# Performance work log

Hardware: AMD Instinct MI355X
Metric: run time of the kernel (lower is better)

Reference implementation:

```python
import jax, jax.numpy as jnp
import numpy as np

NUM_HEADS = 16


def setup_inputs() -> dict:
    key = jax.random.key(0)
    ks = jax.random.split(key, 8)
    B, S, H = 2, 2048, 1024
    sd = 1.0 / np.sqrt(H)
    return {
        "x": jax.random.normal(ks[0], (B, S, H), dtype=jnp.float32),
        "mask": jax.random.randint(ks[1], (B, S), 0, 2, dtype=jnp.int32),
        "wq": jax.random.normal(ks[2], (H, H), dtype=jnp.float32) * sd,
        "bq": jnp.zeros((H,), jnp.float32),
        "wk": jax.random.normal(ks[3], (H, H), dtype=jnp.float32) * sd,
        "bk": jnp.zeros((H,), jnp.float32),
        "wv": jax.random.normal(ks[4], (H, H), dtype=jnp.float32) * sd,
        "bv": jnp.zeros((H,), jnp.float32),
        "wo": jax.random.normal(ks[5], (H, H), dtype=jnp.float32) * sd,
        "bo": jnp.zeros((H,), jnp.float32),
        "wg": jax.random.normal(ks[6], (H, H), dtype=jnp.float32) * sd,
        "bg": jnp.zeros((H,), jnp.float32),
    }


def reference(x, mask, wq, bq, wk, bk, wv, bv, wo, bo, wg, bg):
    B, S, H = x.shape
    nh = NUM_HEADS
    hd = H // nh
    scale = hd ** -0.5

    def split_heads(t):  # [B,S,H] -> [B,nh,S,hd]
        return t.reshape(B, S, nh, hd).transpose(0, 2, 1, 3)

    q = split_heads(x @ wq.T + bq)
    k = split_heads(x @ wk.T + bk)
    v = split_heads(x @ wv.T + bv)

    scores = jnp.einsum("bhqd,bhkd->bhqk", q, k) * scale
    # key-padding mask broadcast to [B,1,1,S]
    scores = jnp.where(mask[:, None, None, :] == 0, jnp.float32(-10000.0), scores)
    attn_weights = jax.nn.softmax(scores, axis=-1)  # dropout is identity in eval

    context = jnp.einsum("bhqk,bhkd->bhqd", attn_weights, v)
    context = context.transpose(0, 2, 1, 3).reshape(B, S, H)

    gate_values = jax.nn.sigmoid(context @ wg.T + bg)
    output = (context @ wo.T + bo) * gate_values
    return output, attn_weights
```

## Files before the change

### kernel.cpp

```cpp
#include <hip/hip_runtime.h>
#include <math.h>

#define BB 2
#define SS 2048
#define HH 1024
#define NH 16
#define HD 64
#define LDK 40

typedef __attribute__((ext_vector_type(8))) short short8;
typedef __attribute__((ext_vector_type(4))) float floatx4;

__device__ __forceinline__ unsigned short f2bf(float f) {
    unsigned u = __float_as_uint(f);
    u += 0x7FFF + ((u >> 16) & 1);
    return (unsigned short)(u >> 16);
}
__device__ __forceinline__ float bf2f(unsigned short h) {
    return __uint_as_float((unsigned)h << 16);
}

struct SplitJob { const float* src; unsigned short* dh; unsigned short* dl; int n; };
struct SplitJobs { SplitJob j[6]; };

__global__ __launch_bounds__(256) void presplit(SplitJobs jobs)
{
    SplitJob jb = jobs.j[blockIdx.y];
    const int i = (blockIdx.x * 256 + threadIdx.x) * 8;
    if (i >= jb.n) return;
    float4 v0 = *(const float4*)(jb.src + i);
    float4 v1 = *(const float4*)(jb.src + i + 4);
    float f[8] = {v0.x, v0.y, v0.z, v0.w, v1.x, v1.y, v1.z, v1.w};
    union { unsigned short s[8]; uint4 v; } h, l;
#pragma unroll
    for (int j = 0; j < 8; ++j) {
        const unsigned short hs = f2bf(f[j]);
        h.s[j] = hs;
        l.s[j] = f2bf(f[j] - bf2f(hs));
    }
    *(uint4*)(jb.dh + i) = h.v;
    *(uint4*)(jb.dl + i) = l.v;
}

__global__ __launch_bounds__(256) void rs_reduce(
    const float* __restrict__ part, float* __restrict__ inv)
{
    const int i = blockIdx.x * 256 + threadIdx.x;
    const int zz = i >> 11, row = i & 2047;
    const float* p = part + (size_t)zz * 32 * SS + row;
    float s = 0.f;
#pragma unroll
    for (int nb = 0; nb < 32; ++nb) s += p[(size_t)nb * SS];
    inv[i] = 1.0f / s;
}

__global__ __launch_bounds__(256) void vtranspose_bf(
    const unsigned short* __restrict__ Vh, const unsigned short* __restrict__ Vl,
    unsigned short* __restrict__ VTh, unsigned short* __restrict__ VTl)
{
    __shared__ __attribute__((aligned(16))) unsigned short t[64][72];
    const int zz = blockIdx.z;
    const int b = zz >> 1;
    const unsigned short* V = (zz & 1) ? Vl : Vh;
    unsigned short* VT = (zz & 1) ? VTl : VTh;
    const int k0 = blockIdx.x * 64;
    const int h = blockIdx.y;
    const int tid = threadIdx.x;
    {
        const int row = tid >> 2, c0 = (tid & 3) * 16;
        const int sw = ((row >> 4) & 3) << 4;
        const unsigned short* g = V + (size_t)(b * SS + k0 + row) * (3 * HH) + h * HD + c0;
        uint4 u0 = *(const uint4*)g;
        uint4 u1 = *(const uint4*)(g + 8);
        *(uint4*)&t[row][c0 ^ sw] = u0;
        *(uint4*)&t[row][(c0 ^ sw) + 8] = u1;
    }
    __syncthreads();
    {
        const int d = tid >> 2, kq = tid & 3;
        const int cs = d ^ (kq << 4);
        union { unsigned short s[16]; uint4 v[2]; } o;
#pragma unroll
        for (int i = 0; i < 16; ++i) o.s[i] = t[kq * 16 + i][cs];
        unsigned short* p = VT + ((size_t)(b * NH + h) * HD + d) * SS + k0 + kq * 16;
        *(uint4*)p = o.v[0];
        *(uint4*)(p + 8) = o.v[1];
    }
}

template<int BN, int MODE>
__global__ __launch_bounds__(256) void gemm_bf(
    const unsigned short* __restrict__ Ah, const unsigned short* __restrict__ Al,
    float* __restrict__ Af,
    const unsigned short* __restrict__ Bh, const unsigned short* __restrict__ Bl,
    const unsigned short* __restrict__ B2h, const unsigned short* __restrict__ B2l,
    const float* __restrict__ bias, const float* __restrict__ bias2, const float* __restrict__ bias3,
    float* __restrict__ Cf, unsigned short* __restrict__ Ch, unsigned short* __restrict__ Cl,
    const float* __restrict__ rs_in, float* __restrict__ rs_out,
    const int* __restrict__ mask,
    int K, int lda, int ldb, int ldc,
    long long sAb, long long sAh, long long sBb, long long sBh,
    long long sCb, long long sCh)
{
    constexpr int BM = 128;
    constexpr int MT = 4;
    constexpr int NT = BN / 32;
    constexpr int NSET = (MODE == 3) ? 2 : 1;

    __shared__ __attribute__((aligned(16))) unsigned short AhS[BM * LDK];
    __shared__ __attribute__((aligned(16))) unsigned short AlS[BM * LDK];
    __shared__ __attribute__((aligned(16))) unsigned short BhS[NSET * BN * LDK];
    __shared__ __attribute__((aligned(16))) unsigned short BlS[NSET * BN * LDK];

    const int tid  = threadIdx.x;
    const int lane = tid & 63;
    const int wave = tid >> 6;
    const int wm = wave >> 1, wn = wave & 1;
    const int r16 = lane & 15, quad = lane >> 4;

    const int z  = blockIdx.z;
    const int bz = z >> 4, hz = z & 15;

    const int m0 = blockIdx.y * BM;
    const int n0 = blockIdx.x * BN;

    floatx4 acc[MT][NT][NSET];
#pragma unroll
    for (int mt = 0; mt < MT; ++mt)
#pragma unroll
        for (int nt = 0; nt < NT; ++nt)
#pragma unroll
            for (int s = 0; s < NSET; ++s)
                acc[mt][nt][s] = (floatx4){0.f, 0.f, 0.f, 0.f};

    const int arow = tid >> 1, ac = (tid & 1) * 16;
    const int brow = (BN == 128) ? (tid >> 1) : (tid >> 2);
    const int bc   = (BN == 128) ? ((tid & 1) * 16) : ((tid & 3) * 8);

    const unsigned short* aph = nullptr;
    const unsigned short* apl = nullptr;
    const unsigned int*   apu = nullptr;
    float* apw = nullptr;
    float invs = 0.f;
    if constexpr (MODE == 2) {
        const size_t zo = (size_t)((long long)bz * sAb + (long long)hz * sAh);
        apu = (const unsigned int*)Af + zo + (size_t)(m0 + arow) * lda + ac;
        apw = Af + zo + (size_t)(m0 + arow) * lda + ac;
        invs = rs_in[(size_t)z * SS + m0 + arow];
    } else {
        const size_t ao = (size_t)((long long)bz * sAb + (long long)hz * sAh)
                        + (size_t)(m0 + arow) * lda + ac;
        aph = Ah + ao;
        apl = Al + ao;
    }
    const size_t boff = (size_t)((long long)bz * sBb + (long long)hz * sBh)
                      + (size_t)(n0 + brow) * ldb + bc;
    const unsigned short* bph = Bh + boff;
    const unsigned short* bpl = Bl + boff;
    const unsigned short* b2ph = nullptr;
    const unsigned short* b2pl = nullptr;
    if constexpr (MODE == 3) {
        const size_t b2o = (size_t)(n0 + brow) * ldb + bc;
        b2ph = B2h + b2o;
        b2pl = B2l + b2o;
    }

    for (int kb = 0; kb < K; kb += 32) {
        uint4 avh0, avh1, avl0, avl1;
        unsigned int uu[16];
        unsigned int hu[8], lu[8];
        uint4 bvh0, bvh1, bvl0, bvl1, cvh0, cvl0;
        if constexpr (MODE == 2) {
            uint4 u0 = *(const uint4*)(apu + kb);
            uint4 u1 = *(const uint4*)(apu + kb + 4);
            uint4 u2 = *(const uint4*)(apu + kb + 8);
            uint4 u3 = *(const uint4*)(apu + kb + 12);
            uu[0]=u0.x;  uu[1]=u0.y;  uu[2]=u0.z;  uu[3]=u0.w;
            uu[4]=u1.x;  uu[5]=u1.y;  uu[6]=u1.z;  uu[7]=u1.w;
            uu[8]=u2.x;  uu[9]=u2.y;  uu[10]=u2.z; uu[11]=u2.w;
            uu[12]=u3.x; uu[13]=u3.y; uu[14]=u3.z; uu[15]=u3.w;
        } else {
            avh0 = *(const uint4*)(aph + kb);
            avh1 = *(const uint4*)(aph + kb + 8);
            avl0 = *(const uint4*)(apl + kb);
            avl1 = *(const uint4*)(apl + kb + 8);
        }
        bvh0 = *(const uint4*)(bph + kb);
        bvl0 = *(const uint4*)(bpl + kb);
        if constexpr (BN == 128) {
            bvh1 = *(const uint4*)(bph + kb + 8);
            bvl1 = *(const uint4*)(bpl + kb + 8);
        }
        if constexpr (MODE == 3) {
            cvh0 = *(const uint4*)(b2ph + kb);
            cvl0 = *(const uint4*)(b2pl + kb);
        }
        if constexpr (MODE == 2) {
#pragma unroll
            for (int i = 0; i < 4; ++i) {
                float4 wv;
                wv.x = (__uint_as_float(uu[4*i+0] << 16) + __uint_as_float(uu[4*i+0] & 0xffff0000u)) * invs;
                wv.y = (__uint_as_float(uu[4*i+1] << 16) + __uint_as_float(uu[4*i+1] & 0xffff0000u)) * invs;
                wv.z = (__uint_as_float(uu[4*i+2] << 16) + __uint_as_float(uu[4*i+2] & 0xffff0000u)) * invs;
                wv.w = (__uint_as_float(uu[4*i+3] << 16) + __uint_as_float(uu[4*i+3] & 0xffff0000u)) * invs;
                *(float4*)(apw + kb + i * 4) = wv;
            }
#pragma unroll
            for (int j = 0; j < 8; ++j) {
                const unsigned int a = uu[2*j], b = uu[2*j+1];
                hu[j] = (a & 0xffffu) | (b << 16);
                lu[j] = (a >> 16) | (b & 0xffff0000u);
            }
        }
        __syncthreads();
        if constexpr (MODE == 2) {
            uint4 t0, t1, t2, t3;
            t0.x=hu[0]; t0.y=hu[1]; t0.z=hu[2]; t0.w=hu[3];
            t1.x=hu[4]; t1.y=hu[5]; t1.z=hu[6]; t1.w=hu[7];
            t2.x=lu[0]; t2.y=lu[1]; t2.z=lu[2]; t2.w=lu[3];
            t3.x=lu[4]; t3.y=lu[5]; t3.z=lu[6]; t3.w=lu[7];
            *(uint4*)&AhS[arow * LDK + ac]     = t0;
            *(uint4*)&AhS[arow * LDK + ac + 8] = t1;
            *(uint4*)&AlS[arow * LDK + ac]     = t2;
            *(uint4*)&AlS[arow * LDK + ac + 8] = t3;
        } else {
            *(uint4*)&AhS[arow * LDK + ac]     = avh0;
            *(uint4*)&AhS[arow * LDK + ac + 8] = avh1;
            *(uint4*)&AlS[arow * LDK + ac]     = avl0;
            *(uint4*)&AlS[arow * LDK + ac + 8] = avl1;
        }
        *(uint4*)&BhS[brow * LDK + bc] = bvh0;
        *(uint4*)&BlS[brow * LDK + bc] = bvl0;
        if constexpr (BN == 128) {
            *(uint4*)&BhS[brow * LDK + bc + 8] = bvh1;
            *(uint4*)&BlS[brow * LDK + bc + 8] = bvl1;
        }
        if constexpr (MODE == 3) {
            *(uint4*)&BhS[BN * LDK + brow * LDK + bc] = cvh0;
            *(uint4*)&BlS[BN * LDK + brow * LDK + bc] = cvl0;
        }
        __syncthreads();

        short8 fah[MT], fal[MT], fbh[NSET][NT], fbl[NSET][NT];
#pragma unroll
        for (int mt = 0; mt < MT; ++mt) {
            const int rr = (wm * 64 + mt * 16 + r16) * LDK + quad * 8;
            fah[mt] = *(const short8*)&AhS[rr];
            fal[mt] = *(const short8*)&AlS[rr];
        }
#pragma unroll
        for (int s = 0; s < NSET; ++s)
#pragma unroll
            for (int nt = 0; nt < NT; ++nt) {
                const int rr = s * BN * LDK + (wn * (BN / 2) + nt * 16 + r16) * LDK + quad * 8;
                fbh[s][nt] = *(const short8*)&BhS[rr];
                fbl[s][nt] = *(const short8*)&BlS[rr];
            }
#pragma unroll
        for (int mt = 0; mt < MT; ++mt)
#pragma unroll
            for (int nt = 0; nt < NT; ++nt)
#pragma unroll
                for (int s = 0; s < NSET; ++s) {
                    acc[mt][nt][s] = __builtin_amdgcn_mfma_f32_16x16x32_bf16(fah[mt], fbh[s][nt], acc[mt][nt][s], 0, 0, 0);
                    acc[mt][nt][s] = __builtin_amdgcn_mfma_f32_16x16x32_bf16(fah[mt], fbl[s][nt], acc[mt][nt][s], 0, 0, 0);
                    acc[mt][nt][s] = __builtin_amdgcn_mfma_f32_16x16x32_bf16(fal[mt], fbh[s][nt], acc[mt][nt][s], 0, 0, 0);
                }
    }

    if constexpr (MODE == 0 || MODE == 2) {
        unsigned short* Chb = Ch + (size_t)((long long)bz * sCb + (long long)hz * sCh);
        unsigned short* Clb = Cl + (size_t)((long long)bz * sCb + (long long)hz * sCh);
#pragma unroll
        for (int nt = 0; nt < NT; ++nt) {
            const int col = n0 + wn * (BN / 2) + nt * 16 + r16;
            float bval = 0.f;
            if constexpr (MODE == 0) {
                const int seg = col >> 10;
                const float* bp = (seg == 0) ? bias : ((seg == 1) ? bias2 : bias3);
                bval = bp[col & (HH - 1)];
            }
#pragma unroll
            for (int mt = 0; mt < MT; ++mt) {
                const int rowb = m0 + wm * 64 + mt * 16 + quad * 4;
#pragma unroll
                for (int r = 0; r < 4; ++r) {
                    float v = acc[mt][nt][0][r];
                    if constexpr (MODE == 0) v += bval;
                    if constexpr (MODE == 2) v *= rs_in[(size_t)z * SS + rowb + r];
                    const unsigned short hv = f2bf(v);
                    const size_t idx = (size_t)(rowb + r) * ldc + col;
                    Chb[idx] = hv;
                    Clb[idx] = f2bf(v - bf2f(hv));
                }
            }
        }
    }
    if constexpr (MODE == 1) {
        unsigned int* Cbu = (unsigned int*)Cf + (size_t)((long long)bz * sCb + (long long)hz * sCh);
        float rsum[MT][4];
#pragma unroll
        for (int mt = 0; mt < MT; ++mt)
#pragma unroll
            for (int r = 0; r < 4; ++r) rsum[mt][r] = 0.f;
#pragma unroll
        for (int nt = 0; nt < NT; ++nt) {
            const int col = n0 + wn * (BN / 2) + nt * 16 + r16;
            const int mv = mask[bz * SS + col];
#pragma unroll
            for (int mt = 0; mt < MT; ++mt) {
                const int rowb = m0 + wm * 64 + mt * 16 + quad * 4;
#pragma unroll
                for (int r = 0; r < 4; ++r) {
                    const float e = mv ? __expf(acc[mt][nt][0][r] * 0.125f) : 0.f;
                    const unsigned short hv = f2bf(e);
                    const unsigned short lv = f2bf(e - bf2f(hv));
                    Cbu[(size_t)(rowb + r) * ldc + col] = (unsigned int)hv | ((unsigned int)lv << 16);
                    rsum[mt][r] += e;
                }
            }
        }
#pragma unroll
        for (int mt = 0; mt < MT; ++mt)
#pragma unroll
            for (int r = 0; r < 4; ++r) {
                float sv = rsum[mt][r];
                sv += __shfl_xor(sv, 1);
                sv += __shfl_xor(sv, 2);
                sv += __shfl_xor(sv, 4);
                sv += __shfl_xor(sv, 8);
                if (r16 == 0)
                    rs_out[((size_t)z * 32 + blockIdx.x * 2 + wn) * SS
                           + (m0 + wm * 64 + mt * 16 + quad * 4 + r)] = sv;
            }
    }
    if constexpr (MODE == 3) {
#pragma unroll
        for (int nt = 0; nt < NT; ++nt) {
            const int col = n0 + wn * (BN / 2) + nt * 16 + r16;
            const float bov = bias[col], bgv = bias2[col];
#pragma unroll
            for (int mt = 0; mt < MT; ++mt) {
                const int rowb = m0 + wm * 64 + mt * 16 + quad * 4;
#pragma unroll
                for (int r = 0; r < 4; ++r) {
                    const float o = acc[mt][nt][0][r] + bov;
                    const float g = acc[mt][nt][1][r] + bgv;
                    Cf[(size_t)(rowb + r) * ldc + col] = o / (1.f + __expf(-g));
                }
            }
        }
    }
}

extern "C" void kernel_launch(void* const* d_in, const int* in_sizes, int n_in,
                              void* d_out, int out_size, void* d_ws, size_t ws_size,
                              hipStream_t stream)
{
    const float* x    = (const float*)d_in[0];
    const int*   mask = (const int*)d_in[1];
    const float* wq = (const float*)d_in[2];  const float* bq = (const float*)d_in[3];
    const float* wk = (const float*)d_in[4];  const float* bk = (const float*)d_in[5];
    const float* wv = (const float*)d_in[6];  const float* bv = (const float*)d_in[7];
    const float* wo = (const float*)d_in[8];  const float* bo = (const float*)d_in[9];
    const float* wg = (const float*)d_in[10]; const float* bg = (const float*)d_in[11];

    const int M = BB * SS;
    const size_t NTOK = (size_t)M * HH;
    const size_t W1   = (size_t)HH * HH;
    const size_t QKVE = (size_t)M * 3 * HH;

    float* out_main = (float*)d_out;
    float* attn     = (float*)d_out + NTOK;

    unsigned short* p = (unsigned short*)d_ws;
    unsigned short* xh   = p;  p += NTOK;
    unsigned short* xl   = p;  p += NTOK;
    unsigned short* Wqh  = p;  p += 3 * W1;
    unsigned short* Wql  = p;  p += 3 * W1;
    unsigned short* Wgh  = p;  p += 2 * W1;
    unsigned short* Wgl  = p;  p += 2 * W1;
    unsigned short* QKVh = p;  p += QKVE;
    unsigned short* QKVl = p;  p += QKVE;
    unsigned short* VTh  = p;  p += NTOK;
    unsigned short* VTl  = p;  p += NTOK;

    unsigned short* CTXh = xh;
    unsigned short* CTXl = xl;
    float* rs_part = (float*)Wqh;
    float* rs_inv  = rs_part + (size_t)32 * 32 * SS;

    SplitJobs jobs;
    jobs.j[0] = SplitJob{x,  xh,           xl,           (int)NTOK};
    jobs.j[1] = SplitJob{wq, Wqh,          Wql,          (int)W1};
    jobs.j[2] = SplitJob{wk, Wqh + W1,     Wql + W1,     (int)W1};
    jobs.j[3] = SplitJob{wv, Wqh + 2 * W1, Wql + 2 * W1, (int)W1};
    jobs.j[4] = SplitJob{wo, Wgh,          Wgl,          (int)W1};
    jobs.j[5] = SplitJob{wg, Wgh + W1,     Wgl + W1,     (int)W1};
    presplit<<<dim3(2048, 6, 1), 256, 0, stream>>>(jobs);

    gemm_bf<128, 0><<<dim3(24, 32, 1), 256, 0, stream>>>(
        xh, xl, nullptr,
        Wqh, Wql, nullptr, nullptr,
        bq, bk, bv,
        nullptr, QKVh, QKVl,
        nullptr, nullptr, nullptr,
        HH, HH, HH, 3 * HH,
        0, 0, 0, 0, 0, 0);

    vtranspose_bf<<<dim3(SS / 64, NH, 2 * BB), 256, 0, stream>>>(
        QKVh + 2 * HH, QKVl + 2 * HH, VTh, VTl);

    gemm_bf<128, 1><<<dim3(16, 16, 32), 256, 0, stream>>>(
        QKVh, QKVl, nullptr,
        QKVh + HH, QKVl + HH, nullptr, nullptr,
        nullptr, nullptr, nullptr,
        attn, nullptr, nullptr,
        nullptr, rs_part, mask,
        HD, 3 * HH, 3 * HH, SS,
        (long long)SS * 3 * HH, HD, (long long)SS * 3 * HH, HD,
        (long long)NH * SS * SS, (long long)SS * SS);

    rs_reduce<<<dim3(32 * SS / 256, 1, 1), 256, 0, stream>>>(rs_part, rs_inv);

    gemm_bf<64, 2><<<dim3(1, 16, 32), 256, 0, stream>>>(
        nullptr, nullptr, attn,
        VTh, VTl, nullptr, nullptr,
        nullptr, nullptr, nullptr,
        nullptr, CTXh, CTXl,
        rs_inv, nullptr, nullptr,
        SS, SS, SS, HH,
        (long long)NH * SS * SS, (long long)SS * SS,
        (long long)NH * HD * SS, (long long)HD * SS,
        (long long)SS * HH, HD);

    gemm_bf<64, 3><<<dim3(16, 32, 1), 256, 0, stream>>>(
        CTXh, CTXl, nullptr,
        Wgh, Wgl, Wgh + W1, Wgl + W1,
        bo, bg, nullptr,
        out_main, nullptr, nullptr,
        nullptr, nullptr, nullptr,
        HH, HH, HH, HH,
        0, 0, 0, 0, 0, 0);

    (void)in_sizes; (void)n_in; (void)out_size; (void)ws_size;
}
```

Before: 1.143 ms.

## Fuse QK^T, softmax and PV into a two-pass attention kernel

```diff
diff --git a/kernel.cpp b/kernel.cpp
--- a/kernel.cpp
+++ b/kernel.cpp
@@ -18,6 +18,11 @@
 }
 __device__ __forceinline__ float bf2f(unsigned short h) {
     return __uint_as_float((unsigned)h << 16);
+}
+__device__ __forceinline__ short8 mkshort8(unsigned d0, unsigned d1, unsigned d2, unsigned d3) {
+    union { unsigned u[4]; short8 s; } t;
+    t.u[0] = d0; t.u[1] = d1; t.u[2] = d2; t.u[3] = d3;
+    return t.s;
 }
 
 struct SplitJob { const float* src; unsigned short* dh; unsigned short* dl; int n; };
@@ -40,18 +45,6 @@
     }
     *(uint4*)(jb.dh + i) = h.v;
     *(uint4*)(jb.dl + i) = l.v;
-}
-
-__global__ __launch_bounds__(256) void rs_reduce(
-    const float* __restrict__ part, float* __restrict__ inv)
-{
-    const int i = blockIdx.x * 256 + threadIdx.x;
-    const int zz = i >> 11, row = i & 2047;
-    const float* p = part + (size_t)zz * 32 * SS + row;
-    float s = 0.f;
-#pragma unroll
-    for (int nb = 0; nb < 32; ++nb) s += p[(size_t)nb * SS];
-    inv[i] = 1.0f / s;
 }
 
 __global__ __launch_bounds__(256) void vtranspose_bf(
@@ -88,19 +81,222 @@
     }
 }
 
+__global__ __launch_bounds__(256) void attn_fused(
+    const unsigned short* __restrict__ QKVh, const unsigned short* __restrict__ QKVl,
+    const unsigned short* __restrict__ VTh, const unsigned short* __restrict__ VTl,
+    const int* __restrict__ mask,
+    float* __restrict__ attn,
+    unsigned short* __restrict__ CTXh, unsigned short* __restrict__ CTXl)
+{
+    __shared__ __attribute__((aligned(16))) unsigned int PS[64 * 64];
+    __shared__ float sums[2][64];
+
+    const int tid = threadIdx.x;
+    const int wave = tid >> 6, lane = tid & 63;
+    const int wm = wave >> 1, wn = wave & 1;
+    const int r16 = lane & 15, quad = lane >> 4;
+
+    const int m0 = blockIdx.x * 64;
+    const int z  = blockIdx.y;
+    const int bz = z >> 4, hz = z & 15;
+
+    short8 fqh[2][2], fql[2][2];
+#pragma unroll
+    for (int mt = 0; mt < 2; ++mt)
+#pragma unroll
+        for (int ks = 0; ks < 2; ++ks) {
+            const size_t off = (size_t)(bz * SS + m0 + wm * 32 + mt * 16 + r16) * (3 * HH)
+                             + hz * HD + ks * 32 + quad * 8;
+            fqh[mt][ks] = *(const short8*)(QKVh + off);
+            fql[mt][ks] = *(const short8*)(QKVl + off);
+        }
+
+    float rsum[2][4];
+#pragma unroll
+    for (int mt = 0; mt < 2; ++mt)
+#pragma unroll
+        for (int r = 0; r < 4; ++r) rsum[mt][r] = 0.f;
+
+    for (int nb = 0; nb < 32; ++nb) {
+        const int kv0 = nb * 64;
+        short8 fkh[2][2], fkl[2][2];
+        int mv[2];
+#pragma unroll
+        for (int nt = 0; nt < 2; ++nt) {
+            const int kvr = kv0 + wn * 32 + nt * 16 + r16;
+            mv[nt] = mask[bz * SS + kvr];
+#pragma unroll
+            for (int ks = 0; ks < 2; ++ks) {
+                const size_t off = (size_t)(bz * SS + kvr) * (3 * HH) + HH + hz * HD
+                                 + ks * 32 + quad * 8;
+                fkh[nt][ks] = *(const short8*)(QKVh + off);
+                fkl[nt][ks] = *(const short8*)(QKVl + off);
+            }
+        }
+        floatx4 p[2][2];
+#pragma unroll
+        for (int mt = 0; mt < 2; ++mt)
+#pragma unroll
+            for (int nt = 0; nt < 2; ++nt) p[mt][nt] = (floatx4){0.f, 0.f, 0.f, 0.f};
+#pragma unroll
+        for (int mt = 0; mt < 2; ++mt)
+#pragma unroll
+            for (int nt = 0; nt < 2; ++nt)
+#pragma unroll
+                for (int ks = 0; ks < 2; ++ks) {
+                    p[mt][nt] = __builtin_amdgcn_mfma_f32_16x16x32_bf16(fqh[mt][ks], fkh[nt][ks], p[mt][nt], 0, 0, 0);
+                    p[mt][nt] = __builtin_amdgcn_mfma_f32_16x16x32_bf16(fqh[mt][ks], fkl[nt][ks], p[mt][nt], 0, 0, 0);
+                    p[mt][nt] = __builtin_amdgcn_mfma_f32_16x16x32_bf16(fql[mt][ks], fkh[nt][ks], p[mt][nt], 0, 0, 0);
+                }
+#pragma unroll
+        for (int mt = 0; mt < 2; ++mt)
+#pragma unroll
+            for (int nt = 0; nt < 2; ++nt)
+#pragma unroll
+                for (int r = 0; r < 4; ++r) {
+                    const float e = mv[nt] ? __expf(p[mt][nt][r] * 0.125f) : 0.f;
+                    rsum[mt][r] += e;
+                }
+    }
+#pragma unroll
+    for (int mt = 0; mt < 2; ++mt)
+#pragma unroll
+        for (int r = 0; r < 4; ++r) {
+            float sv = rsum[mt][r];
+            sv += __shfl_xor(sv, 1); sv += __shfl_xor(sv, 2);
+            sv += __shfl_xor(sv, 4); sv += __shfl_xor(sv, 8);
+            if (r16 == 0) sums[wn][wm * 32 + mt * 16 + quad * 4 + r] = sv;
+        }
+    __syncthreads();
+    float inv[2][4];
+#pragma unroll
+    for (int mt = 0; mt < 2; ++mt)
+#pragma unroll
+        for (int r = 0; r < 4; ++r) {
+            const int row = wm * 32 + mt * 16 + quad * 4 + r;
+            inv[mt][r] = 1.0f / (sums[0][row] + sums[1][row]);
+        }
+
+    floatx4 accc[2][2];
+#pragma unroll
+    for (int mt = 0; mt < 2; ++mt)
+#pragma unroll
+        for (int nt = 0; nt < 2; ++nt) accc[mt][nt] = (floatx4){0.f, 0.f, 0.f, 0.f};
+
+    for (int nb = 0; nb < 32; ++nb) {
+        const int kv0 = nb * 64;
+        short8 fvh[2][2], fvl[2][2];
+#pragma unroll
+        for (int nt = 0; nt < 2; ++nt)
+#pragma unroll
+            for (int kk = 0; kk < 2; ++kk) {
+                const size_t off = ((size_t)z * HD + wn * 32 + nt * 16 + r16) * SS
+                                 + kv0 + kk * 32 + quad * 8;
+                fvh[nt][kk] = *(const short8*)(VTh + off);
+                fvl[nt][kk] = *(const short8*)(VTl + off);
+            }
+        short8 fkh[2][2], fkl[2][2];
+        int mv[2];
+#pragma unroll
+        for (int nt = 0; nt < 2; ++nt) {
+            const int kvr = kv0 + wn * 32 + nt * 16 + r16;
+            mv[nt] = mask[bz * SS + kvr];
+#pragma unroll
+            for (int ks = 0; ks < 2; ++ks) {
+                const size_t off = (size_t)(bz * SS + kvr) * (3 * HH) + HH + hz * HD
+                                 + ks * 32 + quad * 8;
+                fkh[nt][ks] = *(const short8*)(QKVh + off);
+                fkl[nt][ks] = *(const short8*)(QKVl + off);
+            }
+        }
+        floatx4 p[2][2];
+#pragma unroll
+        for (int mt = 0; mt < 2; ++mt)
+#pragma unroll
+            for (int nt = 0; nt < 2; ++nt) p[mt][nt] = (floatx4){0.f, 0.f, 0.f, 0.f};
+#pragma unroll
+        for (int mt = 0; mt < 2; ++mt)
+#pragma unroll
+            for (int nt = 0; nt < 2; ++nt)
+#pragma unroll
+                for (int ks = 0; ks < 2; ++ks) {
+                    p[mt][nt] = __builtin_amdgcn_mfma_f32_16x16x32_bf16(fqh[mt][ks], fkh[nt][ks], p[mt][nt], 0, 0, 0);
+                    p[mt][nt] = __builtin_amdgcn_mfma_f32_16x16x32_bf16(fqh[mt][ks], fkl[nt][ks], p[mt][nt], 0, 0, 0);
+                    p[mt][nt] = __builtin_amdgcn_mfma_f32_16x16x32_bf16(fql[mt][ks], fkh[nt][ks], p[mt][nt], 0, 0, 0);
+                }
+        __syncthreads();
+#pragma unroll
+        for (int nt = 0; nt < 2; ++nt) {
+            const int kvc = wn * 32 + nt * 16 + r16;
+#pragma unroll
+            for (int mt = 0; mt < 2; ++mt) {
+                const int qb = wm * 32 + mt * 16 + quad * 4;
+#pragma unroll
+                for (int r = 0; r < 4; ++r) {
+                    const float e = mv[nt] ? __expf(p[mt][nt][r] * 0.125f) : 0.f;
+                    const float pn = e * inv[mt][r];
+                    attn[((size_t)z * SS + m0 + qb + r) * SS + kv0 + kvc] = pn;
+                    const unsigned short hv = f2bf(pn);
+                    const unsigned short lv = f2bf(pn - bf2f(hv));
+                    const int qrow = qb + r;
+                    PS[qrow * 64 + (kvc ^ ((qrow & 7) << 2))] =
+                        (unsigned)hv | ((unsigned)lv << 16);
+                }
+            }
+        }
+        __syncthreads();
+#pragma unroll
+        for (int mt = 0; mt < 2; ++mt) {
+            const int q = wm * 32 + mt * 16 + r16;
+            const int sw = (q & 7) << 2;
+#pragma unroll
+            for (int kk = 0; kk < 2; ++kk) {
+                const int kvb = kk * 32 + quad * 8;
+                const uint4 a = *(const uint4*)&PS[q * 64 + (kvb ^ sw)];
+                const uint4 b = *(const uint4*)&PS[q * 64 + ((kvb + 4) ^ sw)];
+                const short8 pah = mkshort8((a.x & 0xffffu) | (a.y << 16),
+                                            (a.z & 0xffffu) | (a.w << 16),
+                                            (b.x & 0xffffu) | (b.y << 16),
+                                            (b.z & 0xffffu) | (b.w << 16));
+                const short8 pal = mkshort8((a.x >> 16) | (a.y & 0xffff0000u),
+                                            (a.z >> 16) | (a.w & 0xffff0000u),
+                                            (b.x >> 16) | (b.y & 0xffff0000u),
+                                            (b.z >> 16) | (b.w & 0xffff0000u));
+#pragma unroll
+                for (int nt = 0; nt < 2; ++nt) {
+                    accc[mt][nt] = __builtin_amdgcn_mfma_f32_16x16x32_bf16(pah, fvh[nt][kk], accc[mt][nt], 0, 0, 0);
+                    accc[mt][nt] = __builtin_amdgcn_mfma_f32_16x16x32_bf16(pah, fvl[nt][kk], accc[mt][nt], 0, 0, 0);
+                    accc[mt][nt] = __builtin_amdgcn_mfma_f32_16x16x32_bf16(pal, fvh[nt][kk], accc[mt][nt], 0, 0, 0);
+                }
+            }
+        }
+    }
+#pragma unroll
+    for (int nt = 0; nt < 2; ++nt) {
+        const int dcol = hz * HD + wn * 32 + nt * 16 + r16;
+#pragma unroll
+        for (int mt = 0; mt < 2; ++mt) {
+            const int tok = bz * SS + m0 + wm * 32 + mt * 16 + quad * 4;
+#pragma unroll
+            for (int r = 0; r < 4; ++r) {
+                const float vv = accc[mt][nt][r];
+                const unsigned short hv = f2bf(vv);
+                const size_t idx = (size_t)(tok + r) * HH + dcol;
+                CTXh[idx] = hv;
+                CTXl[idx] = f2bf(vv - bf2f(hv));
+            }
+        }
+    }
+}
+
 template<int BN, int MODE>
 __global__ __launch_bounds__(256) void gemm_bf(
     const unsigned short* __restrict__ Ah, const unsigned short* __restrict__ Al,
-    float* __restrict__ Af,
     const unsigned short* __restrict__ Bh, const unsigned short* __restrict__ Bl,
     const unsigned short* __restrict__ B2h, const unsigned short* __restrict__ B2l,
     const float* __restrict__ bias, const float* __restrict__ bias2, const float* __restrict__ bias3,
     float* __restrict__ Cf, unsigned short* __restrict__ Ch, unsigned short* __restrict__ Cl,
-    const float* __restrict__ rs_in, float* __restrict__ rs_out,
-    const int* __restrict__ mask,
-    int K, int lda, int ldb, int ldc,
-    long long sAb, long long sAh, long long sBb, long long sBh,
-    long long sCb, long long sCh)
+    int K, int lda, int ldb, int ldc)
 {
     constexpr int BM = 128;
     constexpr int MT = 4;
@@ -118,9 +314,6 @@
     const int wm = wave >> 1, wn = wave & 1;
     const int r16 = lane & 15, quad = lane >> 4;
 
-    const int z  = blockIdx.z;
-    const int bz = z >> 4, hz = z & 15;
-
     const int m0 = blockIdx.y * BM;
     const int n0 = blockIdx.x * BN;
 
@@ -137,56 +330,25 @@
     const int brow = (BN == 128) ? (tid >> 1) : (tid >> 2);
     const int bc   = (BN == 128) ? ((tid & 1) * 16) : ((tid & 3) * 8);
 
-    const unsigned short* aph = nullptr;
-    const unsigned short* apl = nullptr;
-    const unsigned int*   apu = nullptr;
-    float* apw = nullptr;
-    float invs = 0.f;
-    if constexpr (MODE == 2) {
-        const size_t zo = (size_t)((long long)bz * sAb + (long long)hz * sAh);
-        apu = (const unsigned int*)Af + zo + (size_t)(m0 + arow) * lda + ac;
-        apw = Af + zo + (size_t)(m0 + arow) * lda + ac;
-        invs = rs_in[(size_t)z * SS + m0 + arow];
-    } else {
-        const size_t ao = (size_t)((long long)bz * sAb + (long long)hz * sAh)
-                        + (size_t)(m0 + arow) * lda + ac;
-        aph = Ah + ao;
-        apl = Al + ao;
-    }
-    const size_t boff = (size_t)((long long)bz * sBb + (long long)hz * sBh)
-                      + (size_t)(n0 + brow) * ldb + bc;
-    const unsigned short* bph = Bh + boff;
-    const unsigned short* bpl = Bl + boff;
+    const unsigned short* aph = Ah + (size_t)(m0 + arow) * lda + ac;
+    const unsigned short* apl = Al + (size_t)(m0 + arow) * lda + ac;
+    const unsigned short* bph = Bh + (size_t)(n0 + brow) * ldb + bc;
+    const unsigned short* bpl = Bl + (size_t)(n0 + brow) * ldb + bc;
     const unsigned short* b2ph = nullptr;
     const unsigned short* b2pl = nullptr;
     if constexpr (MODE == 3) {
-        const size_t b2o = (size_t)(n0 + brow) * ldb + bc;
-        b2ph = B2h + b2o;
-        b2pl = B2l + b2o;
+        b2ph = B2h + (size_t)(n0 + brow) * ldb + bc;
+        b2pl = B2l + (size_t)(n0 + brow) * ldb + bc;
     }
 
     for (int kb = 0; kb < K; kb += 32) {
-        uint4 avh0, avh1, avl0, avl1;
-        unsigned int uu[16];
-        unsigned int hu[8], lu[8];
-        uint4 bvh0, bvh1, bvl0, bvl1, cvh0, cvl0;
-        if constexpr (MODE == 2) {
-            uint4 u0 = *(const uint4*)(apu + kb);
-            uint4 u1 = *(const uint4*)(apu + kb + 4);
-            uint4 u2 = *(const uint4*)(apu + kb + 8);
-            uint4 u3 = *(const uint4*)(apu + kb + 12);
-            uu[0]=u0.x;  uu[1]=u0.y;  uu[2]=u0.z;  uu[3]=u0.w;
-            uu[4]=u1.x;  uu[5]=u1.y;  uu[6]=u1.z;  uu[7]=u1.w;
-            uu[8]=u2.x;  uu[9]=u2.y;  uu[10]=u2.z; uu[11]=u2.w;
-            uu[12]=u3.x; uu[13]=u3.y; uu[14]=u3.z; uu[15]=u3.w;
-        } else {
-            avh0 = *(const uint4*)(aph + kb);
-            avh1 = *(const uint4*)(aph + kb + 8);
-            avl0 = *(const uint4*)(apl + kb);
-            avl1 = *(const uint4*)(apl + kb + 8);
-        }
-        bvh0 = *(const uint4*)(bph + kb);
-        bvl0 = *(const uint4*)(bpl + kb);
+        uint4 avh0 = *(const uint4*)(aph + kb);
+        uint4 avh1 = *(const uint4*)(aph + kb + 8);
+        uint4 avl0 = *(const uint4*)(apl + kb);
+        uint4 avl1 = *(const uint4*)(apl + kb + 8);
+        uint4 bvh0 = *(const uint4*)(bph + kb);
+        uint4 bvl0 = *(const uint4*)(bpl + kb);
+        uint4 bvh1, bvl1, cvh0, cvl0;
         if constexpr (BN == 128) {
             bvh1 = *(const uint4*)(bph + kb + 8);
             bvl1 = *(const uint4*)(bpl + kb + 8);
@@ -195,40 +357,11 @@
             cvh0 = *(const uint4*)(b2ph + kb);
             cvl0 = *(const uint4*)(b2pl + kb);
         }
-        if constexpr (MODE == 2) {
-#pragma unroll
-            for (int i = 0; i < 4; ++i) {
-                float4 wv;
-                wv.x = (__uint_as_float(uu[4*i+0] << 16) + __uint_as_float(uu[4*i+0] & 0xffff0000u)) * invs;
-                wv.y = (__uint_as_float(uu[4*i+1] << 16) + __uint_as_float(uu[4*i+1] & 0xffff0000u)) * invs;
-                wv.z = (__uint_as_float(uu[4*i+2] << 16) + __uint_as_float(uu[4*i+2] & 0xffff0000u)) * invs;
-                wv.w = (__uint_as_float(uu[4*i+3] << 16) + __uint_as_float(uu[4*i+3] & 0xffff0000u)) * invs;
-                *(float4*)(apw + kb + i * 4) = wv;
-            }
-#pragma unroll
-            for (int j = 0; j < 8; ++j) {
-                const unsigned int a = uu[2*j], b = uu[2*j+1];
-                hu[j] = (a & 0xffffu) | (b << 16);
-                lu[j] = (a >> 16) | (b & 0xffff0000u);
-            }
-        }
         __syncthreads();
-        if constexpr (MODE == 2) {
-            uint4 t0, t1, t2, t3;
-            t0.x=hu[0]; t0.y=hu[1]; t0.z=hu[2]; t0.w=hu[3];
-            t1.x=hu[4]; t1.y=hu[5]; t1.z=hu[6]; t1.w=hu[7];
-            t2.x=lu[0]; t2.y=lu[1]; t2.z=lu[2]; t2.w=lu[3];
-            t3.x=lu[4]; t3.y=lu[5]; t3.z=lu[6]; t3.w=lu[7];
-            *(uint4*)&AhS[arow * LDK + ac]     = t0;
-            *(uint4*)&AhS[arow * LDK + ac + 8] = t1;
-            *(uint4*)&AlS[arow * LDK + ac]     = t2;
-            *(uint4*)&AlS[arow * LDK + ac + 8] = t3;
-        } else {
-            *(uint4*)&AhS[arow * LDK + ac]     = avh0;
-            *(uint4*)&AhS[arow * LDK + ac + 8] = avh1;
-            *(uint4*)&AlS[arow * LDK + ac]     = avl0;
-            *(uint4*)&AlS[arow * LDK + ac + 8] = avl1;
-        }
+        *(uint4*)&AhS[arow * LDK + ac]     = avh0;
+        *(uint4*)&AhS[arow * LDK + ac + 8] = avh1;
+        *(uint4*)&AlS[arow * LDK + ac]     = avl0;
+        *(uint4*)&AlS[arow * LDK + ac + 8] = avl1;
         *(uint4*)&BhS[brow * LDK + bc] = bvh0;
         *(uint4*)&BlS[brow * LDK + bc] = bvl0;
         if constexpr (BN == 128) {
@@ -268,71 +401,26 @@
                 }
     }
 
-    if constexpr (MODE == 0 || MODE == 2) {
-        unsigned short* Chb = Ch + (size_t)((long long)bz * sCb + (long long)hz * sCh);
-        unsigned short* Clb = Cl + (size_t)((long long)bz * sCb + (long long)hz * sCh);
+    if constexpr (MODE == 0) {
 #pragma unroll
         for (int nt = 0; nt < NT; ++nt) {
             const int col = n0 + wn * (BN / 2) + nt * 16 + r16;
-            float bval = 0.f;
-            if constexpr (MODE == 0) {
-                const int seg = col >> 10;
-                const float* bp = (seg == 0) ? bias : ((seg == 1) ? bias2 : bias3);
-                bval = bp[col & (HH - 1)];
-            }
+            const int seg = col >> 10;
+            const float* bp = (seg == 0) ? bias : ((seg == 1) ? bias2 : bias3);
+            const float bval = bp[col & (HH - 1)];
 #pragma unroll
             for (int mt = 0; mt < MT; ++mt) {
                 const int rowb = m0 + wm * 64 + mt * 16 + quad * 4;
 #pragma unroll
                 for (int r = 0; r < 4; ++r) {
-                    float v = acc[mt][nt][0][r];
-                    if constexpr (MODE == 0) v += bval;
-                    if constexpr (MODE == 2) v *= rs_in[(size_t)z * SS + rowb + r];
+                    const float v = acc[mt][nt][0][r] + bval;
                     const unsigned short hv = f2bf(v);
                     const size_t idx = (size_t)(rowb + r) * ldc + col;
-                    Chb[idx] = hv;
-                    Clb[idx] = f2bf(v - bf2f(hv));
-                }
-            }
-        }
-    }
-    if constexpr (MODE == 1) {
-        unsigned int* Cbu = (unsigned int*)Cf + (size_t)((long long)bz * sCb + (long long)hz * sCh);
-        float rsum[MT][4];
-#pragma unroll
-        for (int mt = 0; mt < MT; ++mt)
-#pragma unroll
-            for (int r = 0; r < 4; ++r) rsum[mt][r] = 0.f;
-#pragma unroll
-        for (int nt = 0; nt < NT; ++nt) {
-            const int col = n0 + wn * (BN / 2) + nt * 16 + r16;
-            const int mv = mask[bz * SS + col];
-#pragma unroll
-            for (int mt = 0; mt < MT; ++mt) {
-                const int rowb = m0 + wm * 64 + mt * 16 + quad * 4;
-#pragma unroll
-                for (int r = 0; r < 4; ++r) {
-                    const float e = mv ? __expf(acc[mt][nt][0][r] * 0.125f) : 0.f;
-                    const unsigned short hv = f2bf(e);
-                    const unsigned short lv = f2bf(e - bf2f(hv));
-                    Cbu[(size_t)(rowb + r) * ldc + col] = (unsigned int)hv | ((unsigned int)lv << 16);
-                    rsum[mt][r] += e;
-                }
-            }
-        }
-#pragma unroll
-        for (int mt = 0; mt < MT; ++mt)
-#pragma unroll
-            for (int r = 0; r < 4; ++r) {
-                float sv = rsum[mt][r];
-                sv += __shfl_xor(sv, 1);
-                sv += __shfl_xor(sv, 2);
-                sv += __shfl_xor(sv, 4);
-                sv += __shfl_xor(sv, 8);
-                if (r16 == 0)
-                    rs_out[((size_t)z * 32 + blockIdx.x * 2 + wn) * SS
-                           + (m0 + wm * 64 + mt * 16 + quad * 4 + r)] = sv;
-            }
+                    Ch[idx] = hv;
+                    Cl[idx] = f2bf(v - bf2f(hv));
+                }
+            }
+        }
     }
     if constexpr (MODE == 3) {
 #pragma unroll
@@ -387,8 +475,6 @@
 
     unsigned short* CTXh = xh;
     unsigned short* CTXl = xl;
-    float* rs_part = (float*)Wqh;
-    float* rs_inv  = rs_part + (size_t)32 * 32 * SS;
 
     SplitJobs jobs;
     jobs.j[0] = SplitJob{x,  xh,           xl,           (int)NTOK};
@@ -400,48 +486,22 @@
     presplit<<<dim3(2048, 6, 1), 256, 0, stream>>>(jobs);
 
     gemm_bf<128, 0><<<dim3(24, 32, 1), 256, 0, stream>>>(
-        xh, xl, nullptr,
-        Wqh, Wql, nullptr, nullptr,
+        xh, xl, Wqh, Wql, nullptr, nullptr,
         bq, bk, bv,
         nullptr, QKVh, QKVl,
-        nullptr, nullptr, nullptr,
-        HH, HH, HH, 3 * HH,
-        0, 0, 0, 0, 0, 0);
+        HH, HH, HH, 3 * HH);
 
     vtranspose_bf<<<dim3(SS / 64, NH, 2 * BB), 256, 0, stream>>>(
         QKVh + 2 * HH, QKVl + 2 * HH, VTh, VTl);
 
-    gemm_bf<128, 1><<<dim3(16, 16, 32), 256, 0, stream>>>(
-        QKVh, QKVl, nullptr,
-        QKVh + HH, QKVl + HH, nullptr, nullptr,
-        nullptr, nullptr, nullptr,
-        attn, nullptr, nullptr,
-        nullptr, rs_part, mask,
-        HD, 3 * HH, 3 * HH, SS,
-        (long long)SS * 3 * HH, HD, (long long)SS * 3 * HH, HD,
-        (long long)NH * SS * SS, (long long)SS * SS);
-
-    rs_reduce<<<dim3(32 * SS / 256, 1, 1), 256, 0, stream>>>(rs_part, rs_inv);
-
-    gemm_bf<64, 2><<<dim3(1, 16, 32), 256, 0, stream>>>(
-        nullptr, nullptr, attn,
-        VTh, VTl, nullptr, nullptr,
-        nullptr, nullptr, nullptr,
-        nullptr, CTXh, CTXl,
-        rs_inv, nullptr, nullptr,
-        SS, SS, SS, HH,
-        (long long)NH * SS * SS, (long long)SS * SS,
-        (long long)NH * HD * SS, (long long)HD * SS,
-        (long long)SS * HH, HD);
+    attn_fused<<<dim3(SS / 64, BB * NH, 1), 256, 0, stream>>>(
+        QKVh, QKVl, VTh, VTl, mask, attn, CTXh, CTXl);
 
     gemm_bf<64, 3><<<dim3(16, 32, 1), 256, 0, stream>>>(
-        CTXh, CTXl, nullptr,
-        Wgh, Wgl, Wgh + W1, Wgl + W1,
+        CTXh, CTXl, Wgh, Wgl, Wgh + W1, Wgl + W1,
         bo, bg, nullptr,
         out_main, nullptr, nullptr,
-        nullptr, nullptr, nullptr,
-        HH, HH, HH, HH,
-        0, 0, 0, 0, 0, 0);
+        HH, HH, HH, HH);
 
     (void)in_sizes; (void)n_in; (void)out_size; (void)ws_size;
 }
```

Result: faster. 1.104 ms (-3.4%).
